# Kernel tuning notes

Hardware: AMD Instinct MI355X
Metric: run time of the kernel (lower is better)

## Reference

```python
import jax, jax.numpy as jnp
import numpy as np

H, W = 32, 56
CK, CV = 64, 512
N = 16 * H * W  # long + work memory fully populated: 16 frames of H*W entries
TOP_K = 30


def setup_inputs() -> dict:
    key = jax.random.key(0)
    k1, k2, k3, k4, k5 = jax.random.split(key, 5)
    return {
        "q_key": jax.random.normal(k1, (1, CK, H, W), dtype=jnp.float32),
        "q_selection": jax.random.uniform(k2, (1, CK, H, W), dtype=jnp.float32),
        "mem_key": jax.random.normal(k3, (1, CK, N), dtype=jnp.float32),
        "mem_shrinkage": jax.random.uniform(k4, (1, N, 1), dtype=jnp.float32),
        "mem_value": jax.random.normal(k5, (2, CV, N), dtype=jnp.float32),
    }


def reference(q_key, q_selection, mem_key, mem_shrinkage, mem_value):
    b, ck, h, w = q_key.shape
    hw = h * w
    qk = q_key.reshape(1, ck, hw)          # [1, CK, HW]
    qs = q_selection.reshape(1, ck, hw)    # [1, CK, HW]

    mk = jnp.swapaxes(mem_key, 1, 2)       # [1, N, CK]
    # negative weighted squared L2 distance via matmul algebra
    a_sq = jnp.matmul(mk * mk, qs)                    # [1, N, HW]
    two_ab = 2.0 * jnp.matmul(mk, qk * qs)            # [1, N, HW]
    b_sq = jnp.sum(qs * qk * qk, axis=1, keepdims=True)  # [1, 1, HW]
    sim = (-a_sq + two_ab - b_sq) * mem_shrinkage / jnp.sqrt(jnp.float32(ck))  # [1, N, HW]

    # topk over the memory axis (dim=1), softmax over selected entries, scatter back
    simT = jnp.swapaxes(sim, 1, 2)                    # [1, HW, N]
    vals, idx = jax.lax.top_k(simT, TOP_K)            # [1, HW, K]
    x_exp = jnp.exp(vals)
    x_exp = x_exp / jnp.sum(x_exp, axis=-1, keepdims=True)
    i0 = jnp.arange(1)[:, None, None]
    i1 = jnp.arange(hw)[None, :, None]
    affT = jnp.zeros_like(simT).at[i0, i1, idx].set(x_exp)  # [1, HW, N]
    affinity = jnp.swapaxes(affT, 1, 2)               # [1, N, HW]

    out = jnp.matmul(mem_value, affinity)             # [2, CV, HW] (batch-broadcast)
    return out.reshape(2, CV, h, w)
```

## Files before the change

kernel.cpp:

```cpp
#include <hip/hip_runtime.h>
#include <math.h>

#define HW      1792
#define NMEM    28672
#define NCHUNK  3584
#define TOPK    30
#define KSEL    48
#define NCAND   (KSEL * 8)
#define SCAP1   1024
#define SIMB    448
#define WPS     7
#define NSELB   448

typedef __attribute__((ext_vector_type(8))) short bf16x8;
typedef __attribute__((ext_vector_type(8))) unsigned short u16x8;
typedef __attribute__((ext_vector_type(4))) float f32x4;
typedef __attribute__((ext_vector_type(4))) _Float16 h4;
typedef unsigned long long ull;

static __device__ __forceinline__ unsigned short f2bf(float v) {
  unsigned b = __float_as_uint(v);
  return (unsigned short)((b + 0x7FFFu + ((b >> 16) & 1u)) >> 16);
}
static __device__ __forceinline__ float bf2f(unsigned short h) {
  return __uint_as_float(((unsigned)h) << 16);
}
static __device__ __forceinline__ unsigned fkey(float v) {
  return __float_as_uint(-v) & 0x7FFFFFFFu;
}
static __device__ __forceinline__ ull umax64(ull a, ull b) { return a > b ? a : b; }
static __device__ __forceinline__ ull umin64(ull a, ull b) { return a < b ? a : b; }
static __device__ __forceinline__ void gl_lds16(const void* g, void* l) {
  __builtin_amdgcn_global_load_lds(
      (const __attribute__((address_space(1))) unsigned*)g,
      (__attribute__((address_space(3))) unsigned*)l, 16, 0, 0);
}
#define WSYNC() do { asm volatile("s_waitcnt lgkmcnt(0)" ::: "memory"); \
                     __builtin_amdgcn_wave_barrier(); } while (0)

__global__ __launch_bounds__(256)
void k_prep_b(const float* __restrict__ mk, const float* __restrict__ shr_in,
              unsigned short* __restrict__ Bh,
              float* __restrict__ mkT, float* __restrict__ shr_s)
{
  const int n = blockIdx.x * 256 + threadIdx.x;
  shr_s[n] = shr_in[n] * 0.125f;
  for (int cb = 0; cb < 64; cb += 8) {
    u16x8 h1, h2;
    float vv[8];
    #pragma unroll
    for (int j = 0; j < 8; ++j) {
      float v = mk[(size_t)(cb + j) * NMEM + n];
      vv[j] = v;
      h1[j] = f2bf(v);
      h2[j] = f2bf(v * v);
    }
    const int s = cb >> 3;
    *reinterpret_cast<u16x8*>(&Bh[((size_t)s * NMEM + n) * 8])       = h1;
    *reinterpret_cast<u16x8*>(&Bh[((size_t)(s + 8) * NMEM + n) * 8]) = h2;
    *reinterpret_cast<float4*>(&mkT[(size_t)n * 64 + cb])     = make_float4(vv[0], vv[1], vv[2], vv[3]);
    *reinterpret_cast<float4*>(&mkT[(size_t)n * 64 + cb + 4]) = make_float4(vv[4], vv[5], vv[6], vv[7]);
  }
}

__global__ __launch_bounds__(256)
void k_prep_u(const float* __restrict__ q_key, const float* __restrict__ q_sel,
              unsigned short* __restrict__ Uh, unsigned short* __restrict__ Ul,
              float* __restrict__ bsq)
{
  const int p = blockIdx.x * 256 + threadIdx.x;
  float bs = 0.f;
  for (int cb = 0; cb < 64; cb += 8) {
    u16x8 h1, l1, h2, l2;
    #pragma unroll
    for (int j = 0; j < 8; ++j) {
      int c = cb + j;
      float k = q_key[(size_t)c * HW + p];
      float s = q_sel[(size_t)c * HW + p];
      float u = 2.f * k * s;
      float w = -s;
      bs = fmaf(s * k, k, bs);
      unsigned short h = f2bf(u); h1[j] = h; l1[j] = f2bf(u - bf2f(h));
      unsigned short g = f2bf(w); h2[j] = g; l2[j] = f2bf(w - bf2f(g));
    }
    const int s = cb >> 3;
    *reinterpret_cast<u16x8*>(&Uh[((size_t)s * HW + p) * 8])       = h1;
    *reinterpret_cast<u16x8*>(&Ul[((size_t)s * HW + p) * 8])       = l1;
    *reinterpret_cast<u16x8*>(&Uh[((size_t)(s + 8) * HW + p) * 8]) = h2;
    *reinterpret_cast<u16x8*>(&Ul[((size_t)(s + 8) * HW + p) * 8]) = l2;
  }
  bsq[p] = bs;
}

__global__ __launch_bounds__(256, 2)
void k_sim(const unsigned short* __restrict__ Uh, const unsigned short* __restrict__ Ul,
           const unsigned short* __restrict__ Bh,
           const float* __restrict__ bsq, const float* __restrict__ shr_s,
           float* __restrict__ pmax)
{
  __shared__ char smem[65536] __attribute__((aligned(16)));
  const int tid = threadIdx.x;
  const int wid = tid >> 6, lane = tid & 63;
  const int lr = lane & 15, lg = lane >> 4;
  const int pb = blockIdx.x % 14, st = blockIdx.x / 14;
  const int pw = pb * 128 + wid * 32;
  const int w0 = st * WPS;

  bf16x8 a0h[4], a0l[4], a1h[4], a1l[4];
  #pragma unroll
  for (int t = 0; t < 4; ++t) {
    const size_t e0 = ((size_t)(t * 4 + lg) * HW + pw + lr) * 8;
    const size_t e1 = e0 + 16 * 8;
    a0h[t] = *reinterpret_cast<const bf16x8*>(&Uh[e0]);
    a0l[t] = *reinterpret_cast<const bf16x8*>(&Ul[e0]);
    a1h[t] = *reinterpret_cast<const bf16x8*>(&Uh[e1]);
    a1l[t] = *reinterpret_cast<const bf16x8*>(&Ul[e1]);
  }
  float bq[2][4];
  #pragma unroll
  for (int pt = 0; pt < 2; ++pt)
    #pragma unroll
    for (int r = 0; r < 4; ++r) bq[pt][r] = bsq[pw + pt * 16 + 4 * lg + r];

  auto stage = [&](int buf, int i) {
    const int n0 = (w0 + i) * 128;
    #pragma unroll
    for (int j = 0; j < 8; ++j) {
      const int idx = j * 256 + tid;
      const int s = idx >> 7, rr = idx & 127;
      gl_lds16((const char*)Bh + ((size_t)s * NMEM + n0 + rr) * 16,
               smem + buf * 32768 + idx * 16);
    }
  };

  stage(0, 0);
  int buf = 0;
  for (int i = 0; i < WPS; ++i) {
    __syncthreads();
    if (i + 1 < WPS) stage(buf ^ 1, i + 1);

    f32x4 acc[2][8];
    #pragma unroll
    for (int a = 0; a < 2; ++a)
      #pragma unroll
      for (int b = 0; b < 8; ++b) acc[a][b] = (f32x4){0.f, 0.f, 0.f, 0.f};

    const short* lb = (const short*)(smem + buf * 32768);
    #pragma unroll
    for (int t = 0; t < 4; ++t) {
      #pragma unroll
      for (int nt = 0; nt < 8; ++nt) {
        bf16x8 bh = *reinterpret_cast<const bf16x8*>(
            &lb[((t * 4 + lg) * 128 + nt * 16 + lr) * 8]);
        acc[0][nt] = __builtin_amdgcn_mfma_f32_16x16x32_bf16(a0h[t], bh, acc[0][nt], 0, 0, 0);
        acc[0][nt] = __builtin_amdgcn_mfma_f32_16x16x32_bf16(a0l[t], bh, acc[0][nt], 0, 0, 0);
        acc[1][nt] = __builtin_amdgcn_mfma_f32_16x16x32_bf16(a1h[t], bh, acc[1][nt], 0, 0, 0);
        acc[1][nt] = __builtin_amdgcn_mfma_f32_16x16x32_bf16(a1l[t], bh, acc[1][nt], 0, 0, 0);
      }
    }

    const int wgl = w0 + i;
    const int n0 = wgl * 128;
    float shv[8];
    #pragma unroll
    for (int nt = 0; nt < 8; ++nt) shv[nt] = shr_s[n0 + nt * 16 + lr];
    #pragma unroll
    for (int pt = 0; pt < 2; ++pt) {
      #pragma unroll
      for (int r = 0; r < 4; ++r) {
        float mx = -INFINITY;
        #pragma unroll
        for (int nt = 0; nt < 8; ++nt)
          mx = fmaxf(mx, (acc[pt][nt][r] - bq[pt][r]) * shv[nt]);
        pmax[(size_t)(pw + pt * 16 + 4 * lg + r) * NCHUNK + wgl * 16 + lr] = mx;
      }
    }
    buf ^= 1;
  }
}

struct SelS {
  ull   buf[4][SCAP1];
  short sl[4][KSEL];
  float sqk[4][64], sqs[4][64];
};
union SMemU { SelS sel; float tt[64][65]; };

__global__ __launch_bounds__(256, 4)
void k_selT(const float* __restrict__ pmax, const float* __restrict__ mkT,
            const float* __restrict__ q_key, const float* __restrict__ q_sel,
            const float* __restrict__ shr_s,
            float* __restrict__ wgt, int* __restrict__ widx,
            const float* __restrict__ mv, _Float16* __restrict__ mvT)
{
  __shared__ SMemU sm;
  const int tid = threadIdx.x;

  int sg = -1, tb = -1;
  if (gridDim.x > NSELB) {
    const int g = blockIdx.x / 17, r = blockIdx.x % 17;
    if (r == 0) sg = g; else tb = g * 16 + (r - 1);
  } else {
    sg = blockIdx.x;
  }

  if (tb >= 0) {
    const int n0 = (tb % 448) * 64, ch0 = (tb / 448) * 64;
    for (int i = tid; i < 64 * 16; i += 256) {
      int r = i >> 4, c4 = (i & 15) << 2;
      float4 v = *reinterpret_cast<const float4*>(&mv[(size_t)(ch0 + r) * NMEM + n0 + c4]);
      sm.tt[r][c4] = v.x; sm.tt[r][c4 + 1] = v.y;
      sm.tt[r][c4 + 2] = v.z; sm.tt[r][c4 + 3] = v.w;
    }
    __syncthreads();
    for (int i = tid; i < 64 * 16; i += 256) {
      int r = i >> 4, c4 = (i & 15) << 2;
      h4 hv = {(_Float16)sm.tt[c4][r], (_Float16)sm.tt[c4 + 1][r],
               (_Float16)sm.tt[c4 + 2][r], (_Float16)sm.tt[c4 + 3][r]};
      *reinterpret_cast<h4*>(&mvT[(size_t)(n0 + r) * 1024 + ch0 + c4]) = hv;
    }
    return;
  }

  const int w = tid >> 6, lane = tid & 63;
  const int pix = sg * 4 + w;
  ull*   buf  = sm.sel.buf[w];
  ull*   cand = buf;
  ull*   fin  = buf + NCAND;
  short* sl   = sm.sel.sl[w];

  sm.sel.sqk[w][lane] = q_key[(size_t)lane * HW + pix];
  sm.sel.sqs[w][lane] = q_sel[(size_t)lane * HW + pix];

  const float* pm = pmax + (size_t)pix * NCHUNK;

  float mx = -INFINITY;
  #pragma unroll
  for (int j = 0; j < 56; ++j) mx = fmaxf(mx, pm[lane + 64 * j]);

  float v = mx;
  #pragma unroll
  for (int k = 2; k <= 64; k <<= 1) {
    #pragma unroll
    for (int j = k >> 1; j > 0; j >>= 1) {
      float o = __shfl_xor(v, j);
      bool keepmin = (((lane & k) == 0) == ((lane & j) == 0));
      v = keepmin ? fminf(v, o) : fmaxf(v, o);
    }
  }
  const float t0 = __shfl(v, 64 - KSEL);

  int ns0 = 0;
  #pragma unroll
  for (int j = 0; j < 56; ++j) {
    float mv2 = pm[lane + 64 * j];
    bool keep = (mv2 >= t0);
    ull ball = __ballot(keep);
    if (keep) {
      int pos = ns0 + __popcll(ball & ((1ull << lane) - 1ull));
      if (pos < SCAP1)
        buf[pos] = ((ull)(0x7FFFFFFFu - fkey(mv2)) << 32) | (unsigned)(lane + 64 * j);
    }
    ns0 += __popcll(ball);
  }
  ns0 = (ns0 < SCAP1) ? ns0 : SCAP1;
  WSYNC();

  {
    ull e0 = (lane < ns0) ? buf[lane] : 0ull;
    ull e1 = (lane + 64 < ns0) ? buf[lane + 64] : 0ull;
    int r0 = 0, r1 = 0;
    for (int k = 0; k < ns0; ++k) {
      ull kb = buf[k];
      r0 += (kb > e0); r1 += (kb > e1);
    }
    if (e0 && r0 < KSEL) sl[r0] = (short)(unsigned)(e0 & 0xFFFFu);
    if (e1 && r1 < KSEL) sl[r1] = (short)(unsigned)(e1 & 0xFFFFu);
    for (int base = 128; base < ns0; base += 64) {
      ull ee = (base + lane < ns0) ? buf[base + lane] : 0ull;
      int rr = 0;
      for (int k = 0; k < ns0; ++k) rr += (buf[k] > ee);
      if (ee && rr < KSEL) sl[rr] = (short)(unsigned)(ee & 0xFFFFu);
    }
  }
  WSYNC();

  const float4* k4p = reinterpret_cast<const float4*>(sm.sel.sqk[w]);
  const float4* s4p = reinterpret_cast<const float4*>(sm.sel.sqs[w]);
  ull myp[6];
  #pragma unroll
  for (int i = 0; i < 6; ++i) {
    const int c = lane + (i << 6);
    const int cc = sl[c >> 3];
    const int n = ((cc >> 4) << 7) + (cc & 15) + ((c & 7) << 4);
    const float4* mr = reinterpret_cast<const float4*>(mkT + (size_t)n * 64);
    float s0 = 0.f, s1 = 0.f, s2 = 0.f, s3 = 0.f;
    #pragma unroll
    for (int j = 0; j < 4; ++j) {
      float4 q0 = mr[4*j], q1 = mr[4*j+1], q2 = mr[4*j+2], q3 = mr[4*j+3];
      float4 a0 = k4p[4*j], a1 = k4p[4*j+1], a2 = k4p[4*j+2], a3 = k4p[4*j+3];
      float4 b0 = s4p[4*j], b1 = s4p[4*j+1], b2 = s4p[4*j+2], b3 = s4p[4*j+3];
      float d;
      d = q0.x-a0.x; s0 = fmaf(b0.x*d, d, s0);
      d = q0.y-a0.y; s1 = fmaf(b0.y*d, d, s1);
      d = q0.z-a0.z; s2 = fmaf(b0.z*d, d, s2);
      d = q0.w-a0.w; s3 = fmaf(b0.w*d, d, s3);
      d = q1.x-a1.x; s0 = fmaf(b1.x*d, d, s0);
      d = q1.y-a1.y; s1 = fmaf(b1.y*d, d, s1);
      d = q1.z-a1.z; s2 = fmaf(b1.z*d, d, s2);
      d = q1.w-a1.w; s3 = fmaf(b1.w*d, d, s3);
      d = q2.x-a2.x; s0 = fmaf(b2.x*d, d, s0);
      d = q2.y-a2.y; s1 = fmaf(b2.y*d, d, s1);
      d = q2.z-a2.z; s2 = fmaf(b2.z*d, d, s2);
      d = q2.w-a2.w; s3 = fmaf(b2.w*d, d, s3);
      d = q3.x-a3.x; s0 = fmaf(b3.x*d, d, s0);
      d = q3.y-a3.y; s1 = fmaf(b3.y*d, d, s1);
      d = q3.z-a3.z; s2 = fmaf(b3.z*d, d, s2);
      d = q3.w-a3.w; s3 = fmaf(b3.w*d, d, s3);
    }
    float sv = -((s0 + s1) + (s2 + s3)) * shr_s[n];
    ull pk = ((ull)(0x7FFFFFFFu - fkey(sv)) << 32) |
             (ull)(0xFFFFFFFFu - (unsigned)n);
    cand[c] = pk;
    myp[i] = pk;
  }
  WSYNC();

  ull p0 = 0, p1 = 0, p2 = 0, p3 = 0;
  #pragma unroll
  for (int i = 0; i < 6; ++i) {
    ull k = myp[i], m;
    m = umax64(p0, k); k = umin64(p0, k); p0 = m;
    m = umax64(p1, k); k = umin64(p1, k); p1 = m;
    m = umax64(p2, k); k = umin64(p2, k); p2 = m;
    m = umax64(p3, k); k = umin64(p3, k); p3 = m;
  }
  fin[lane * 4 + 0] = p0; fin[lane * 4 + 1] = p1;
  fin[lane * 4 + 2] = p2; fin[lane * 4 + 3] = p3;
  WSYNC();

  int r0 = 0, r1 = 0, r2 = 0, r3 = 0;
  for (int k = 0; k < 256; ++k) {
    ull kb = fin[k];
    r0 += (kb > p0); r1 += (kb > p1); r2 += (kb > p2); r3 += (kb > p3);
  }
  ull c30 = (r0 == TOPK - 1) ? p0 : (r1 == TOPK - 1) ? p1 :
            (r2 == TOPK - 1) ? p2 : (r3 == TOPK - 1) ? p3 : 0ull;
  ull ball = __ballot(c30 != 0ull);
  ull k30 = __shfl(c30, (int)(__ffsll((long long)ball) - 1));

  int cnt = 0;
  #pragma unroll
  for (int i = 0; i < 6; ++i) cnt += (myp[i] > k30);
  #pragma unroll
  for (int off = 32; off > 0; off >>= 1) cnt += __shfl_xor(cnt, off);
  const bool ok = (cnt == TOPK - 1);

  if (ok) {
    float v0 = -__uint_as_float(0x7FFFFFFFu - (unsigned)(p0 >> 32));
    float v1 = -__uint_as_float(0x7FFFFFFFu - (unsigned)(p1 >> 32));
    float v2 = -__uint_as_float(0x7FFFFFFFu - (unsigned)(p2 >> 32));
    float v3 = -__uint_as_float(0x7FFFFFFFu - (unsigned)(p3 >> 32));
    float e0 = (r0 < TOPK) ? expf(v0) : 0.f;
    float e1 = (r1 < TOPK) ? expf(v1) : 0.f;
    float e2 = (r2 < TOPK) ? expf(v2) : 0.f;
    float e3 = (r3 < TOPK) ? expf(v3) : 0.f;
    float es = e0 + e1 + e2 + e3;
    #pragma unroll
    for (int off = 32; off > 0; off >>= 1) es += __shfl_xor(es, off);
    if (r0 < TOPK) { wgt[(size_t)pix*32 + r0] = e0/es; widx[(size_t)pix*32 + r0] = (int)(0xFFFFFFFFu - (unsigned)(p0 & 0xFFFFFFFFu)); }
    if (r1 < TOPK) { wgt[(size_t)pix*32 + r1] = e1/es; widx[(size_t)pix*32 + r1] = (int)(0xFFFFFFFFu - (unsigned)(p1 & 0xFFFFFFFFu)); }
    if (r2 < TOPK) { wgt[(size_t)pix*32 + r2] = e2/es; widx[(size_t)pix*32 + r2] = (int)(0xFFFFFFFFu - (unsigned)(p2 & 0xFFFFFFFFu)); }
    if (r3 < TOPK) { wgt[(size_t)pix*32 + r3] = e3/es; widx[(size_t)pix*32 + r3] = (int)(0xFFFFFFFFu - (unsigned)(p3 & 0xFFFFFFFFu)); }
  } else {
    int rr[6];
    #pragma unroll
    for (int i = 0; i < 6; ++i) rr[i] = 0;
    for (int k = 0; k < NCAND; ++k) {
      ull kb = cand[k];
      #pragma unroll
      for (int i = 0; i < 6; ++i) rr[i] += (kb > myp[i]);
    }
    float ev[6]; float es = 0.f;
    #pragma unroll
    for (int i = 0; i < 6; ++i) {
      float vv = -__uint_as_float(0x7FFFFFFFu - (unsigned)(myp[i] >> 32));
      ev[i] = (rr[i] < TOPK) ? expf(vv) : 0.f;
      es += ev[i];
    }
    #pragma unroll
    for (int off = 32; off > 0; off >>= 1) es += __shfl_xor(es, off);
    #pragma unroll
    for (int i = 0; i < 6; ++i) {
      if (rr[i] < TOPK) {
        wgt [(size_t)pix * 32 + rr[i]] = ev[i] / es;
        widx[(size_t)pix * 32 + rr[i]] = (int)(0xFFFFFFFFu - (unsigned)(myp[i] & 0xFFFFFFFFu));
      }
    }
  }
}

__global__ __launch_bounds__(256)
void k_transpose_h(const float* __restrict__ mv, _Float16* __restrict__ mvT)
{
  __shared__ float t[64][65];
  const int n0 = blockIdx.x * 64, ch0 = blockIdx.y * 64;
  const int tid = threadIdx.x;
  for (int i = tid; i < 64 * 16; i += 256) {
    int r = i >> 4, c4 = (i & 15) << 2;
    float4 v = *reinterpret_cast<const float4*>(&mv[(size_t)(ch0 + r) * NMEM + n0 + c4]);
    t[r][c4] = v.x; t[r][c4 + 1] = v.y; t[r][c4 + 2] = v.z; t[r][c4 + 3] = v.w;
  }
  __syncthreads();
  for (int i = tid; i < 64 * 16; i += 256) {
    int r = i >> 4, c4 = (i & 15) << 2;
    h4 hv = {(_Float16)t[c4][r], (_Float16)t[c4 + 1][r],
             (_Float16)t[c4 + 2][r], (_Float16)t[c4 + 3][r]};
    *reinterpret_cast<h4*>(&mvT[(size_t)(n0 + r) * 1024 + ch0 + c4]) = hv;
  }
}

__global__ __launch_bounds__(256)
void k_gather_h(const _Float16* __restrict__ mvT, const float* __restrict__ wgt,
                const int* __restrict__ widx, float* __restrict__ out)
{
  __shared__ float sw[8][TOPK];
  __shared__ int   si[8][TOPK];
  __shared__ float sbuf[256][9];
  const int p0 = blockIdx.x * 8, chg = blockIdx.y * 256;
  const int tid = threadIdx.x;

  for (int i = tid; i < 8 * TOPK; i += 256) {
    int q = i / TOPK, k = i - q * TOPK;
    sw[q][k] = wgt [(size_t)(p0 + q) * 32 + k];
    si[q][k] = widx[(size_t)(p0 + q) * 32 + k];
  }
  __syncthreads();

  const int ch = chg + tid;
  #pragma unroll 2
  for (int q = 0; q < 8; ++q) {
    float a = 0.f;
    #pragma unroll
    for (int k = 0; k < TOPK; ++k)
      a = fmaf(sw[q][k], (float)mvT[(size_t)si[q][k] * 1024 + ch], a);
    sbuf[tid][q] = a;
  }
  __syncthreads();

  for (int i = tid; i < 256 * 8; i += 256) {
    int cl = i >> 3, q = i & 7;
    out[(size_t)(chg + cl) * HW + p0 + q] = sbuf[cl][q];
  }
}

__global__ __launch_bounds__(256)
void k_gather_f(const float* __restrict__ src, const float* __restrict__ wgt,
                const int* __restrict__ widx, float* __restrict__ out,
                long n_stride, long ch_stride)
{
  __shared__ float sw[8][TOPK];
  __shared__ int   si[8][TOPK];
  __shared__ float sbuf[256][9];
  const int p0 = blockIdx.x * 8, chg = blockIdx.y * 256;
  const int tid = threadIdx.x;

  for (int i = tid; i < 8 * TOPK; i += 256) {
    int q = i / TOPK, k = i - q * TOPK;
    sw[q][k] = wgt [(size_t)(p0 + q) * 32 + k];
    si[q][k] = widx[(size_t)(p0 + q) * 32 + k];
  }
  __syncthreads();

  const int ch = chg + tid;
  #pragma unroll 2
  for (int q = 0; q < 8; ++q) {
    float a = 0.f;
    #pragma unroll
    for (int k = 0; k < TOPK; ++k)
      a = fmaf(sw[q][k], src[(size_t)si[q][k] * n_stride + (size_t)ch * ch_stride], a);
    sbuf[tid][q] = a;
  }
  __syncthreads();

  for (int i = tid; i < 256 * 8; i += 256) {
    int cl = i >> 3, q = i & 7;
    out[(size_t)(chg + cl) * HW + p0 + q] = sbuf[cl][q];
  }
}

extern "C" void kernel_launch(void* const* d_in, const int* in_sizes, int n_in,
                              void* d_out, int out_size, void* d_ws, size_t ws_size,
                              hipStream_t stream)
{
  (void)in_sizes; (void)n_in; (void)out_size;
  const float* q_key     = (const float*)d_in[0];
  const float* q_sel     = (const float*)d_in[1];
  const float* mem_key   = (const float*)d_in[2];
  const float* mem_shr   = (const float*)d_in[3];
  const float* mem_value = (const float*)d_in[4];
  float* out = (float*)d_out;

  char* ws = (char*)d_ws;
  size_t off = 0;
  auto alloc = [&](size_t b) { size_t c = off; off = (off + b + 255) & ~(size_t)255; return c; };
  size_t o_w   = alloc((size_t)HW * 32 * 4);
  size_t o_wi  = alloc((size_t)HW * 32 * 4);
  size_t o_pr  = off;
  size_t o_bh  = alloc((size_t)NMEM * 128 * 2);
  size_t o_uh  = alloc((size_t)HW * 128 * 2);
  size_t o_ul  = alloc((size_t)HW * 128 * 2);
  size_t o_bsq = alloc((size_t)HW * 4);
  size_t o_shr = alloc((size_t)NMEM * 4);
  size_t o_mkT = alloc((size_t)NMEM * 64 * 4);
  size_t o_pm  = alloc((size_t)HW * NCHUNK * 4);
  size_t o_end = off;

  float*          wg   = (float*)(ws + o_w);
  int*            wi   = (int*)  (ws + o_wi);
  unsigned short* Bh   = (unsigned short*)(ws + o_bh);
  unsigned short* Uh   = (unsigned short*)(ws + o_uh);
  unsigned short* Ul   = (unsigned short*)(ws + o_ul);
  float*          bsq  = (float*)(ws + o_bsq);
  float*          shr  = (float*)(ws + o_shr);
  float*          mkT  = (float*)(ws + o_mkT);
  float*          pmx  = (float*)(ws + o_pm);

  const size_t mvh_sz = (size_t)NMEM * 1024 * 2;

  k_prep_b<<<NMEM / 256, 256, 0, stream>>>(mem_key, mem_shr, Bh, mkT, shr);
  k_prep_u<<<HW / 256, 256, 0, stream>>>(q_key, q_sel, Uh, Ul, bsq);
  k_sim<<<SIMB, 256, 0, stream>>>(Uh, Ul, Bh, bsq, shr, pmx);

  if (ws_size >= o_end + mvh_sz) {
    _Float16* mvT = (_Float16*)(ws + o_end);
    k_selT<<<NSELB * 17, 256, 0, stream>>>(pmx, mkT, q_key, q_sel, shr,
                                           wg, wi, mem_value, mvT);
    k_gather_h<<<dim3(HW / 8, 4), 256, 0, stream>>>(mvT, wg, wi, out);
  } else if (ws_size >= o_pr + mvh_sz) {
    k_selT<<<NSELB, 256, 0, stream>>>(pmx, mkT, q_key, q_sel, shr,
                                      wg, wi, mem_value, nullptr);
    _Float16* mvT = (_Float16*)(ws + o_pr);
    k_transpose_h<<<dim3(NMEM / 64, 16), 256, 0, stream>>>(mem_value, mvT);
    k_gather_h<<<dim3(HW / 8, 4), 256, 0, stream>>>(mvT, wg, wi, out);
  } else {
    k_selT<<<NSELB, 256, 0, stream>>>(pmx, mkT, q_key, q_sel, shr,
                                      wg, wi, mem_value, nullptr);
    k_gather_f<<<dim3(HW / 8, 4), 256, 0, stream>>>(
        mem_value, wg, wi, out, 1, NMEM);
  }
}
```

Measured before the change: 169.7 us.

## Replace chunk-max sort with radix binary-search threshold and unfuse transpose from select

The chunk-max preselection now holds all 56 per-lane keys in registers and binary-searches the exact 48th threshold with a warp-wide count. This replaces the bitonic estimate, the up-to-1024-entry candidate buffer and the O(n^2) rank pass, so at most 64 chunks are kept and candidate evaluation scales with the actual count. The value transpose is split back out of the select kernel into its own launch before selection, which drops the shared-memory union and lowers the occupancy hint. The trade-off is about 31 serial search iterations with shuffle reductions, more registers, and one extra kernel launch that no longer overlaps with the select work.

```diff
diff --git a/kernel.cpp b/kernel.cpp
--- a/kernel.cpp
+++ b/kernel.cpp
@@ -6,11 +6,9 @@
 #define NCHUNK  3584
 #define TOPK    30
 #define KSEL    48
-#define NCAND   (KSEL * 8)
-#define SCAP1   1024
+#define SCAP    64
 #define SIMB    448
 #define WPS     7
-#define NSELB   448
 
 typedef __attribute__((ext_vector_type(8))) short bf16x8;
 typedef __attribute__((ext_vector_type(8))) unsigned short u16x8;
@@ -179,179 +177,127 @@
   }
 }
 
-struct SelS {
-  ull   buf[4][SCAP1];
-  short sl[4][KSEL];
-  float sqk[4][64], sqs[4][64];
-};
-union SMemU { SelS sel; float tt[64][65]; };
-
-__global__ __launch_bounds__(256, 4)
-void k_selT(const float* __restrict__ pmax, const float* __restrict__ mkT,
-            const float* __restrict__ q_key, const float* __restrict__ q_sel,
-            const float* __restrict__ shr_s,
-            float* __restrict__ wgt, int* __restrict__ widx,
-            const float* __restrict__ mv, _Float16* __restrict__ mvT)
-{
-  __shared__ SMemU sm;
-  const int tid = threadIdx.x;
-
-  int sg = -1, tb = -1;
-  if (gridDim.x > NSELB) {
-    const int g = blockIdx.x / 17, r = blockIdx.x % 17;
-    if (r == 0) sg = g; else tb = g * 16 + (r - 1);
-  } else {
-    sg = blockIdx.x;
-  }
-
-  if (tb >= 0) {
-    const int n0 = (tb % 448) * 64, ch0 = (tb / 448) * 64;
-    for (int i = tid; i < 64 * 16; i += 256) {
-      int r = i >> 4, c4 = (i & 15) << 2;
-      float4 v = *reinterpret_cast<const float4*>(&mv[(size_t)(ch0 + r) * NMEM + n0 + c4]);
-      sm.tt[r][c4] = v.x; sm.tt[r][c4 + 1] = v.y;
-      sm.tt[r][c4 + 2] = v.z; sm.tt[r][c4 + 3] = v.w;
-    }
-    __syncthreads();
-    for (int i = tid; i < 64 * 16; i += 256) {
-      int r = i >> 4, c4 = (i & 15) << 2;
-      h4 hv = {(_Float16)sm.tt[c4][r], (_Float16)sm.tt[c4 + 1][r],
-               (_Float16)sm.tt[c4 + 2][r], (_Float16)sm.tt[c4 + 3][r]};
-      *reinterpret_cast<h4*>(&mvT[(size_t)(n0 + r) * 1024 + ch0 + c4]) = hv;
-    }
-    return;
-  }
-
-  const int w = tid >> 6, lane = tid & 63;
-  const int pix = sg * 4 + w;
-  ull*   buf  = sm.sel.buf[w];
-  ull*   cand = buf;
-  ull*   fin  = buf + NCAND;
-  short* sl   = sm.sel.sl[w];
-
-  sm.sel.sqk[w][lane] = q_key[(size_t)lane * HW + pix];
-  sm.sel.sqs[w][lane] = q_sel[(size_t)lane * HW + pix];
-
+__global__ __launch_bounds__(256, 2)
+void k_select(const float* __restrict__ pmax, const float* __restrict__ mkT,
+              const float* __restrict__ q_key, const float* __restrict__ q_sel,
+              const float* __restrict__ shr_s,
+              float* __restrict__ wgt, int* __restrict__ widx)
+{
+  __shared__ ull   cand[4][512];
+  __shared__ ull   fin[4][256];
+  __shared__ short sl[4][SCAP];
+  __shared__ float sqk[4][64], sqs[4][64];
+
+  const int w = threadIdx.x >> 6, lane = threadIdx.x & 63;
+  const int pix = blockIdx.x * 4 + w;
+  ull*   cd = cand[w];
+  ull*   fn = fin[w];
+  short* sv = sl[w];
+
+  sqk[w][lane] = q_key[(size_t)lane * HW + pix];
+  sqs[w][lane] = q_sel[(size_t)lane * HW + pix];
+
+  unsigned kk[56];
   const float* pm = pmax + (size_t)pix * NCHUNK;
-
-  float mx = -INFINITY;
-  #pragma unroll
-  for (int j = 0; j < 56; ++j) mx = fmaxf(mx, pm[lane + 64 * j]);
-
-  float v = mx;
-  #pragma unroll
-  for (int k = 2; k <= 64; k <<= 1) {
-    #pragma unroll
-    for (int j = k >> 1; j > 0; j >>= 1) {
-      float o = __shfl_xor(v, j);
-      bool keepmin = (((lane & k) == 0) == ((lane & j) == 0));
-      v = keepmin ? fminf(v, o) : fmaxf(v, o);
-    }
-  }
-  const float t0 = __shfl(v, 64 - KSEL);
-
-  int ns0 = 0;
+  #pragma unroll
+  for (int j = 0; j < 56; ++j) kk[j] = fkey(pm[lane + 64 * j]);
+
+  unsigned lo = 0, hi = 0x7FFFFFFFu;
+  while (lo < hi) {
+    unsigned mid = (lo + hi) >> 1;
+    int c = 0;
+    #pragma unroll
+    for (int j = 0; j < 56; ++j) c += (kk[j] <= mid);
+    #pragma unroll
+    for (int off = 1; off < 64; off <<= 1) c += __shfl_xor(c, off);
+    if (c >= KSEL) hi = mid; else lo = mid + 1;
+  }
+  const unsigned T48 = lo;
+
+  int ns = 0;
   #pragma unroll
   for (int j = 0; j < 56; ++j) {
-    float mv2 = pm[lane + 64 * j];
-    bool keep = (mv2 >= t0);
+    bool keep = (kk[j] <= T48);
     ull ball = __ballot(keep);
     if (keep) {
-      int pos = ns0 + __popcll(ball & ((1ull << lane) - 1ull));
-      if (pos < SCAP1)
-        buf[pos] = ((ull)(0x7FFFFFFFu - fkey(mv2)) << 32) | (unsigned)(lane + 64 * j);
-    }
-    ns0 += __popcll(ball);
-  }
-  ns0 = (ns0 < SCAP1) ? ns0 : SCAP1;
+      int pos = ns + __popcll(ball & ((1ull << lane) - 1ull));
+      if (pos < SCAP) sv[pos] = (short)(lane + 64 * j);
+    }
+    ns += __popcll(ball);
+  }
+  ns = (ns < SCAP) ? ns : SCAP;
+  const int NC = ns * 8;
   WSYNC();
 
-  {
-    ull e0 = (lane < ns0) ? buf[lane] : 0ull;
-    ull e1 = (lane + 64 < ns0) ? buf[lane + 64] : 0ull;
-    int r0 = 0, r1 = 0;
-    for (int k = 0; k < ns0; ++k) {
-      ull kb = buf[k];
-      r0 += (kb > e0); r1 += (kb > e1);
-    }
-    if (e0 && r0 < KSEL) sl[r0] = (short)(unsigned)(e0 & 0xFFFFu);
-    if (e1 && r1 < KSEL) sl[r1] = (short)(unsigned)(e1 & 0xFFFFu);
-    for (int base = 128; base < ns0; base += 64) {
-      ull ee = (base + lane < ns0) ? buf[base + lane] : 0ull;
-      int rr = 0;
-      for (int k = 0; k < ns0; ++k) rr += (buf[k] > ee);
-      if (ee && rr < KSEL) sl[rr] = (short)(unsigned)(ee & 0xFFFFu);
-    }
+  const float4* k4p = reinterpret_cast<const float4*>(sqk[w]);
+  const float4* s4p = reinterpret_cast<const float4*>(sqs[w]);
+  ull myp[8];
+  #pragma unroll
+  for (int i = 0; i < 8; ++i) {
+    myp[i] = 0ull;
+    const int c = lane + (i << 6);
+    if (c < NC) {
+      const int cc = sv[c >> 3];
+      const int n = ((cc >> 4) << 7) + (cc & 15) + ((c & 7) << 4);
+      const float4* mr = reinterpret_cast<const float4*>(mkT + (size_t)n * 64);
+      float s0 = 0.f, s1 = 0.f, s2 = 0.f, s3 = 0.f;
+      #pragma unroll
+      for (int j = 0; j < 4; ++j) {
+        float4 q0 = mr[4*j], q1 = mr[4*j+1], q2 = mr[4*j+2], q3 = mr[4*j+3];
+        float4 a0 = k4p[4*j], a1 = k4p[4*j+1], a2 = k4p[4*j+2], a3 = k4p[4*j+3];
+        float4 b0 = s4p[4*j], b1 = s4p[4*j+1], b2 = s4p[4*j+2], b3 = s4p[4*j+3];
+        float d;
+        d = q0.x-a0.x; s0 = fmaf(b0.x*d, d, s0);
+        d = q0.y-a0.y; s1 = fmaf(b0.y*d, d, s1);
+        d = q0.z-a0.z; s2 = fmaf(b0.z*d, d, s2);
+        d = q0.w-a0.w; s3 = fmaf(b0.w*d, d, s3);
+        d = q1.x-a1.x; s0 = fmaf(b1.x*d, d, s0);
+        d = q1.y-a1.y; s1 = fmaf(b1.y*d, d, s1);
+        d = q1.z-a1.z; s2 = fmaf(b1.z*d, d, s2);
+        d = q1.w-a1.w; s3 = fmaf(b1.w*d, d, s3);
+        d = q2.x-a2.x; s0 = fmaf(b2.x*d, d, s0);
+        d = q2.y-a2.y; s1 = fmaf(b2.y*d, d, s1);
+        d = q2.z-a2.z; s2 = fmaf(b2.z*d, d, s2);
+        d = q2.w-a2.w; s3 = fmaf(b2.w*d, d, s3);
+        d = q3.x-a3.x; s0 = fmaf(b3.x*d, d, s0);
+        d = q3.y-a3.y; s1 = fmaf(b3.y*d, d, s1);
+        d = q3.z-a3.z; s2 = fmaf(b3.z*d, d, s2);
+        d = q3.w-a3.w; s3 = fmaf(b3.w*d, d, s3);
+      }
+      float svv = -((s0 + s1) + (s2 + s3)) * shr_s[n];
+      myp[i] = ((ull)(0x7FFFFFFFu - fkey(svv)) << 32) |
+               (ull)(0xFFFFFFFFu - (unsigned)n);
+    }
+    cd[lane + (i << 6)] = myp[i];
   }
   WSYNC();
 
-  const float4* k4p = reinterpret_cast<const float4*>(sm.sel.sqk[w]);
-  const float4* s4p = reinterpret_cast<const float4*>(sm.sel.sqs[w]);
-  ull myp[6];
-  #pragma unroll
-  for (int i = 0; i < 6; ++i) {
-    const int c = lane + (i << 6);
-    const int cc = sl[c >> 3];
-    const int n = ((cc >> 4) << 7) + (cc & 15) + ((c & 7) << 4);
-    const float4* mr = reinterpret_cast<const float4*>(mkT + (size_t)n * 64);
-    float s0 = 0.f, s1 = 0.f, s2 = 0.f, s3 = 0.f;
-    #pragma unroll
-    for (int j = 0; j < 4; ++j) {
-      float4 q0 = mr[4*j], q1 = mr[4*j+1], q2 = mr[4*j+2], q3 = mr[4*j+3];
-      float4 a0 = k4p[4*j], a1 = k4p[4*j+1], a2 = k4p[4*j+2], a3 = k4p[4*j+3];
-      float4 b0 = s4p[4*j], b1 = s4p[4*j+1], b2 = s4p[4*j+2], b3 = s4p[4*j+3];
-      float d;
-      d = q0.x-a0.x; s0 = fmaf(b0.x*d, d, s0);
-      d = q0.y-a0.y; s1 = fmaf(b0.y*d, d, s1);
-      d = q0.z-a0.z; s2 = fmaf(b0.z*d, d, s2);
-      d = q0.w-a0.w; s3 = fmaf(b0.w*d, d, s3);
-      d = q1.x-a1.x; s0 = fmaf(b1.x*d, d, s0);
-      d = q1.y-a1.y; s1 = fmaf(b1.y*d, d, s1);
-      d = q1.z-a1.z; s2 = fmaf(b1.z*d, d, s2);
-      d = q1.w-a1.w; s3 = fmaf(b1.w*d, d, s3);
-      d = q2.x-a2.x; s0 = fmaf(b2.x*d, d, s0);
-      d = q2.y-a2.y; s1 = fmaf(b2.y*d, d, s1);
-      d = q2.z-a2.z; s2 = fmaf(b2.z*d, d, s2);
-      d = q2.w-a2.w; s3 = fmaf(b2.w*d, d, s3);
-      d = q3.x-a3.x; s0 = fmaf(b3.x*d, d, s0);
-      d = q3.y-a3.y; s1 = fmaf(b3.y*d, d, s1);
-      d = q3.z-a3.z; s2 = fmaf(b3.z*d, d, s2);
-      d = q3.w-a3.w; s3 = fmaf(b3.w*d, d, s3);
-    }
-    float sv = -((s0 + s1) + (s2 + s3)) * shr_s[n];
-    ull pk = ((ull)(0x7FFFFFFFu - fkey(sv)) << 32) |
-             (ull)(0xFFFFFFFFu - (unsigned)n);
-    cand[c] = pk;
-    myp[i] = pk;
-  }
-  WSYNC();
-
   ull p0 = 0, p1 = 0, p2 = 0, p3 = 0;
   #pragma unroll
-  for (int i = 0; i < 6; ++i) {
+  for (int i = 0; i < 8; ++i) {
     ull k = myp[i], m;
     m = umax64(p0, k); k = umin64(p0, k); p0 = m;
     m = umax64(p1, k); k = umin64(p1, k); p1 = m;
     m = umax64(p2, k); k = umin64(p2, k); p2 = m;
     m = umax64(p3, k); k = umin64(p3, k); p3 = m;
   }
-  fin[lane * 4 + 0] = p0; fin[lane * 4 + 1] = p1;
-  fin[lane * 4 + 2] = p2; fin[lane * 4 + 3] = p3;
+  fn[lane * 4 + 0] = p0; fn[lane * 4 + 1] = p1;
+  fn[lane * 4 + 2] = p2; fn[lane * 4 + 3] = p3;
   WSYNC();
 
   int r0 = 0, r1 = 0, r2 = 0, r3 = 0;
   for (int k = 0; k < 256; ++k) {
-    ull kb = fin[k];
+    ull kb = fn[k];
     r0 += (kb > p0); r1 += (kb > p1); r2 += (kb > p2); r3 += (kb > p3);
   }
   ull c30 = (r0 == TOPK - 1) ? p0 : (r1 == TOPK - 1) ? p1 :
             (r2 == TOPK - 1) ? p2 : (r3 == TOPK - 1) ? p3 : 0ull;
-  ull ball = __ballot(c30 != 0ull);
-  ull k30 = __shfl(c30, (int)(__ffsll((long long)ball) - 1));
+  ull ball2 = __ballot(c30 != 0ull);
+  ull k30 = __shfl(c30, (int)(__ffsll((long long)ball2) - 1));
 
   int cnt = 0;
   #pragma unroll
-  for (int i = 0; i < 6; ++i) cnt += (myp[i] > k30);
+  for (int i = 0; i < 8; ++i) cnt += (myp[i] > k30);
   #pragma unroll
   for (int off = 32; off > 0; off >>= 1) cnt += __shfl_xor(cnt, off);
   const bool ok = (cnt == TOPK - 1);
@@ -373,26 +319,26 @@
     if (r2 < TOPK) { wgt[(size_t)pix*32 + r2] = e2/es; widx[(size_t)pix*32 + r2] = (int)(0xFFFFFFFFu - (unsigned)(p2 & 0xFFFFFFFFu)); }
     if (r3 < TOPK) { wgt[(size_t)pix*32 + r3] = e3/es; widx[(size_t)pix*32 + r3] = (int)(0xFFFFFFFFu - (unsigned)(p3 & 0xFFFFFFFFu)); }
   } else {
-    int rr[6];
-    #pragma unroll
-    for (int i = 0; i < 6; ++i) rr[i] = 0;
-    for (int k = 0; k < NCAND; ++k) {
-      ull kb = cand[k];
+    int rr[8];
+    #pragma unroll
+    for (int i = 0; i < 8; ++i) rr[i] = 0;
+    for (int k = 0; k < NC; ++k) {
+      ull kb = cd[k];
       #pragma unroll
-      for (int i = 0; i < 6; ++i) rr[i] += (kb > myp[i]);
-    }
-    float ev[6]; float es = 0.f;
-    #pragma unroll
-    for (int i = 0; i < 6; ++i) {
+      for (int i = 0; i < 8; ++i) rr[i] += (kb > myp[i]);
+    }
+    float ev[8]; float es = 0.f;
+    #pragma unroll
+    for (int i = 0; i < 8; ++i) {
       float vv = -__uint_as_float(0x7FFFFFFFu - (unsigned)(myp[i] >> 32));
-      ev[i] = (rr[i] < TOPK) ? expf(vv) : 0.f;
+      ev[i] = (myp[i] != 0ull && rr[i] < TOPK) ? expf(vv) : 0.f;
       es += ev[i];
     }
     #pragma unroll
     for (int off = 32; off > 0; off >>= 1) es += __shfl_xor(es, off);
     #pragma unroll
-    for (int i = 0; i < 6; ++i) {
-      if (rr[i] < TOPK) {
+    for (int i = 0; i < 8; ++i) {
+      if (myp[i] != 0ull && rr[i] < TOPK) {
         wgt [(size_t)pix * 32 + rr[i]] = ev[i] / es;
         widx[(size_t)pix * 32 + rr[i]] = (int)(0xFFFFFFFFu - (unsigned)(myp[i] & 0xFFFFFFFFu));
       }
@@ -534,18 +480,16 @@
 
   if (ws_size >= o_end + mvh_sz) {
     _Float16* mvT = (_Float16*)(ws + o_end);
-    k_selT<<<NSELB * 17, 256, 0, stream>>>(pmx, mkT, q_key, q_sel, shr,
-                                           wg, wi, mem_value, mvT);
+    k_transpose_h<<<dim3(NMEM / 64, 16), 256, 0, stream>>>(mem_value, mvT);
+    k_select<<<HW / 4, 256, 0, stream>>>(pmx, mkT, q_key, q_sel, shr, wg, wi);
     k_gather_h<<<dim3(HW / 8, 4), 256, 0, stream>>>(mvT, wg, wi, out);
   } else if (ws_size >= o_pr + mvh_sz) {
-    k_selT<<<NSELB, 256, 0, stream>>>(pmx, mkT, q_key, q_sel, shr,
-                                      wg, wi, mem_value, nullptr);
+    k_select<<<HW / 4, 256, 0, stream>>>(pmx, mkT, q_key, q_sel, shr, wg, wi);
     _Float16* mvT = (_Float16*)(ws + o_pr);
     k_transpose_h<<<dim3(NMEM / 64, 16), 256, 0, stream>>>(mem_value, mvT);
     k_gather_h<<<dim3(HW / 8, 4), 256, 0, stream>>>(mvT, wg, wi, out);
   } else {
-    k_selT<<<NSELB, 256, 0, stream>>>(pmx, mkT, q_key, q_sel, shr,
-                                      wg, wi, mem_value, nullptr);
+    k_select<<<HW / 4, 256, 0, stream>>>(pmx, mkT, q_key, q_sel, shr, wg, wi);
     k_gather_f<<<dim3(HW / 8, 4), 256, 0, stream>>>(
         mem_value, wg, wi, out, 1, NMEM);
   }
```

New measurement: 150.2 us. 11.5% less time.
